# Performance work log

Hardware: AMD Instinct MI355X
Metric: run time of the kernel (lower is better)

The kernel has to match this reference:

```python
import jax, jax.numpy as jnp
import numpy as np

B, T, S, H = 4, 128, 512, 256


def setup_inputs() -> dict:
    key = jax.random.key(0)
    k0, k1, k2, k3, k4, k5, k6 = jax.random.split(key, 7)
    query = jax.random.normal(k0, (B, T, H), dtype=jnp.float32)
    encoder_outputs = jax.random.normal(k1, (B, S, H), dtype=jnp.float32)
    src_lengths = jax.random.randint(k2, (B,), 1, S + 1).astype(jnp.int32)
    # torch code's mask assumes max(src_lengths) == S (src dim of encoder_outputs)
    src_lengths = src_lengths.at[0].set(S)
    sc = np.float32(1.0 / np.sqrt(H))
    Ws = jax.random.normal(k3, (H, H), dtype=jnp.float32) * sc      # nn.Linear(H,H).weight
    Wh = jax.random.normal(k4, (H, H), dtype=jnp.float32) * sc
    v = jax.random.normal(k5, (H,), dtype=jnp.float32) * sc         # nn.Linear(H,1).weight squeezed
    Wout = jax.random.normal(k6, (H, 2 * H), dtype=jnp.float32) * sc
    return {"query": query, "encoder_outputs": encoder_outputs, "src_lengths": src_lengths,
            "Ws": Ws, "Wh": Wh, "v": v, "Wout": Wout}


def reference(query, encoder_outputs, src_lengths, Ws, Wh, v, Wout):
    # projections: torch Linear is x @ W.T
    pq = jnp.einsum('bth,oh->bto', query, Ws)             # (B,T,H)
    pe = jnp.einsum('bsh,oh->bso', encoder_outputs, Wh)   # (B,S,H)
    # additive score: v^T tanh(Ws q + Wh h) -> (B,T,S)
    e = jnp.einsum('btsh,h->bts', jnp.tanh(pq[:, :, None, :] + pe[:, None, :, :]), v)
    s = encoder_outputs.shape[1]
    mask = jnp.arange(s)[None, :] < src_lengths[:, None]  # (B,S) True = valid
    e = jnp.where(mask[:, None, :], e, -jnp.inf)
    alpha = jax.nn.softmax(e, axis=-1)                    # (B,T,S)
    c = jnp.einsum('bts,bsh->bth', alpha, encoder_outputs)  # context (B,T,H)
    cat = jnp.concatenate([query, c], axis=-1)            # (B,T,2H)
    attn_out = jnp.tanh(jnp.einsum('btf,of->bto', cat, Wout))
    return attn_out
```

## Files before the change

kernel.cpp:

```cpp
#include <hip/hip_runtime.h>
#include <math.h>

#define NB 4
#define NT 128
#define NS 512
#define NH 256

#define SCALE_2LOG2E 2.8853900817779268f

__device__ __forceinline__ float fast_exp2(float x) {
#if __has_builtin(__builtin_amdgcn_exp2f)
    return __builtin_amdgcn_exp2f(x);
#else
    return __expf(x * 0.6931471805599453f);
#endif
}

__device__ __forceinline__ float fast_tanh(float x) {
    float e = __expf(2.0f * x);
    return 1.0f - 2.0f / (e + 1.0f);
}

__device__ __forceinline__ float dot4(float4 a, float4 b, float acc) {
    acc = fmaf(a.x, b.x, acc);
    acc = fmaf(a.y, b.y, acc);
    acc = fmaf(a.z, b.z, acc);
    acc = fmaf(a.w, b.w, acc);
    return acc;
}

__device__ __forceinline__ void gemm_tile_64x64(
    float4* __restrict__ wsh, float4* __restrict__ xsh,
    const float* __restrict__ Wp, int wstride,
    const float* __restrict__ Xp,
    int kchunks, int tid, float acc[4][4])
{
    const int o0 = (tid & 15) * 4;
    const int m0 = (tid >> 4) * 4;
    const int srow = tid >> 2, sjl = tid & 3;
    const int wslotx = (tid & 7);
    const int xslotx = ((tid >> 4) & 7);

    for (int ck = 0; ck < kchunks; ++ck) {
        __syncthreads();
        {
            const float4* src = reinterpret_cast<const float4*>(
                Wp + (size_t)srow * wstride + ck * 128);
            const int rsw = (srow >> 2) & 7;
#pragma unroll
            for (int k = 0; k < 8; ++k) {
                const int j = sjl + 4 * k;
                wsh[srow * 32 + ((j & 31) ^ rsw)] = src[j];
            }
        }
        {
            const float4* src = reinterpret_cast<const float4*>(
                Xp + (size_t)srow * NH + ck * 128);
            const int rsw = (srow >> 2) & 7;
#pragma unroll
            for (int k = 0; k < 8; ++k) {
                const int j = sjl + 4 * k;
                xsh[srow * 32 + ((j & 31) ^ rsw)] = src[j];
            }
        }
        __syncthreads();

#pragma unroll 4
        for (int k4 = 0; k4 < 32; ++k4) {
            float4 wv0 = wsh[(o0 + 0) * 32 + (k4 ^ wslotx)];
            float4 wv1 = wsh[(o0 + 1) * 32 + (k4 ^ wslotx)];
            float4 wv2 = wsh[(o0 + 2) * 32 + (k4 ^ wslotx)];
            float4 wv3 = wsh[(o0 + 3) * 32 + (k4 ^ wslotx)];
            float4 xv0 = xsh[(m0 + 0) * 32 + (k4 ^ xslotx)];
            float4 xv1 = xsh[(m0 + 1) * 32 + (k4 ^ xslotx)];
            float4 xv2 = xsh[(m0 + 2) * 32 + (k4 ^ xslotx)];
            float4 xv3 = xsh[(m0 + 3) * 32 + (k4 ^ xslotx)];
            acc[0][0] = dot4(xv0, wv0, acc[0][0]);
            acc[0][1] = dot4(xv0, wv1, acc[0][1]);
            acc[0][2] = dot4(xv0, wv2, acc[0][2]);
            acc[0][3] = dot4(xv0, wv3, acc[0][3]);
            acc[1][0] = dot4(xv1, wv0, acc[1][0]);
            acc[1][1] = dot4(xv1, wv1, acc[1][1]);
            acc[1][2] = dot4(xv1, wv2, acc[1][2]);
            acc[1][3] = dot4(xv1, wv3, acc[1][3]);
            acc[2][0] = dot4(xv2, wv0, acc[2][0]);
            acc[2][1] = dot4(xv2, wv1, acc[2][1]);
            acc[2][2] = dot4(xv2, wv2, acc[2][2]);
            acc[2][3] = dot4(xv2, wv3, acc[2][3]);
            acc[3][0] = dot4(xv3, wv0, acc[3][0]);
            acc[3][1] = dot4(xv3, wv1, acc[3][1]);
            acc[3][2] = dot4(xv3, wv2, acc[3][2]);
            acc[3][3] = dot4(xv3, wv3, acc[3][3]);
        }
    }
}

__global__ __launch_bounds__(256) void kA_proj(
    const float* __restrict__ enc, const float* __restrict__ q,
    const float* __restrict__ Wh, const float* __restrict__ Ws,
    const float* __restrict__ Wout, const float* __restrict__ v,
    float4* __restrict__ peP, float* __restrict__ pq,
    float* __restrict__ oq, float* __restrict__ w2t, float* __restrict__ w)
{
    __shared__ float4 wsh[64 * 32];
    __shared__ float4 xsh[64 * 32];

    const int bx = blockIdx.x;
    const int tid = threadIdx.x;

    if (bx >= 192) {
        float* tl = reinterpret_cast<float*>(wsh);
        const int bi = bx - 192;
        const int oi = bi & 3, ki = bi >> 2;
        const int row = tid >> 2, jl = tid & 3;
        {
            const float4* src = reinterpret_cast<const float4*>(
                Wout + (size_t)(oi * 64 + row) * (2 * NH) + NH + ki * 64);
#pragma unroll
            for (int kk = 0; kk < 4; ++kk) {
                const int j = jl + 4 * kk;
                const float4 val = src[j];
                tl[(4 * j + 0) * 65 + row] = val.x;
                tl[(4 * j + 1) * 65 + row] = val.y;
                tl[(4 * j + 2) * 65 + row] = val.z;
                tl[(4 * j + 3) * 65 + row] = val.w;
            }
        }
        __syncthreads();
        {
#pragma unroll
            for (int kk = 0; kk < 4; ++kk) {
                const int j = jl + 4 * kk;
                float4 val;
                val.x = tl[row * 65 + 4 * j + 0];
                val.y = tl[row * 65 + 4 * j + 1];
                val.z = tl[row * 65 + 4 * j + 2];
                val.w = tl[row * 65 + 4 * j + 3];
                reinterpret_cast<float4*>(
                    w2t + (size_t)(ki * 64 + row) * NH + oi * 64)[j] = val;
            }
        }
        return;
    }

    float acc[4][4];
#pragma unroll
    for (int i = 0; i < 4; ++i)
#pragma unroll
        for (int j = 0; j < 4; ++j) acc[i][j] = 0.f;

    if (bx == 128) w[tid] = -2.0f * v[tid];

    const int o0 = (tid & 15) * 4;
    const int m0 = (tid >> 4) * 4;

    if (bx < 128) {
        const int mt = bx >> 2, ot = bx & 3;
        const int m_base = mt * 64;
        gemm_tile_64x64(wsh, xsh, Wh + (size_t)(ot * 64) * NH, NH,
                        enc + (size_t)m_base * NH, 2, tid, acc);
        const int b = m_base >> 9, s_base = m_base & (NS - 1);
        const int quad = ot * 16 + (tid & 15);
#pragma unroll
        for (int i = 0; i < 4; ++i) {
            peP[(size_t)(b * 64 + quad) * NS + s_base + m0 + i] =
                make_float4(acc[i][0] * SCALE_2LOG2E, acc[i][1] * SCALE_2LOG2E,
                            acc[i][2] * SCALE_2LOG2E, acc[i][3] * SCALE_2LOG2E);
        }
    } else if (bx < 160) {
        const int bi = bx - 128;
        const int mt = bi >> 2, ot = bi & 3;
        const int m_base = mt * 64;
        gemm_tile_64x64(wsh, xsh, Ws + (size_t)(ot * 64) * NH, NH,
                        q + (size_t)m_base * NH, 2, tid, acc);
#pragma unroll
        for (int i = 0; i < 4; ++i) {
            *reinterpret_cast<float4*>(
                pq + (size_t)(m_base + m0 + i) * NH + ot * 64 + o0) =
                make_float4(acc[i][0] * SCALE_2LOG2E, acc[i][1] * SCALE_2LOG2E,
                            acc[i][2] * SCALE_2LOG2E, acc[i][3] * SCALE_2LOG2E);
        }
    } else {
        const int bi = bx - 160;
        const int mt = bi >> 2, ot = bi & 3;
        const int m_base = mt * 64;
        gemm_tile_64x64(wsh, xsh, Wout + (size_t)(ot * 64) * (2 * NH), 2 * NH,
                        q + (size_t)m_base * NH, 2, tid, acc);
#pragma unroll
        for (int i = 0; i < 4; ++i) {
            *reinterpret_cast<float4*>(
                oq + (size_t)(m_base + m0 + i) * NH + ot * 64 + o0) =
                make_float4(acc[i][0], acc[i][1], acc[i][2], acc[i][3]);
        }
    }
}

__global__ __launch_bounds__(512) void kB_score(
    const float4* __restrict__ peP, const float* __restrict__ pq,
    const float* __restrict__ w, float* __restrict__ e)
{
    __shared__ float4 pp[64 * 64];
    __shared__ float4 pqs[16 * 64];
    __shared__ float4 wls[64];

    const int sx = blockIdx.x;
    const int ty = blockIdx.y;
    const int b  = blockIdx.z;
    const int tid = threadIdx.x;
    const int t0 = ty * 16;

    {
        const int row = tid >> 3, jl = tid & 7;
        const float4* src = peP + (size_t)(b * 64 + row) * NS + sx * 64;
#pragma unroll
        for (int k = 0; k < 8; ++k) pp[row * 64 + jl + 8 * k] = src[jl + 8 * k];
    }
    {
        const int r = tid >> 5, j = tid & 31;
        const float4* src = reinterpret_cast<const float4*>(
            pq + (size_t)(b * NT + t0 + r) * NH);
        pqs[r * 64 + j] = src[j];
        pqs[r * 64 + j + 32] = src[j + 32];
    }
    if (tid < 64) wls[tid] = reinterpret_cast<const float4*>(w)[tid];
    __syncthreads();

    const int lane = tid & 63;
    const int wvi  = tid >> 6;
    const int tA = wvi, tB = wvi + 8;

    float a0 = 0.f, a1 = 0.f, a2 = 0.f, a3 = 0.f;
    float b0 = 0.f, b1 = 0.f, b2 = 0.f, b3 = 0.f;
#pragma unroll 4
    for (int h4 = 0; h4 < 64; ++h4) {
        const float4 pv = pp[h4 * 64 + lane];
        const float4 qa = pqs[tA * 64 + h4];
        const float4 qb = pqs[tB * 64 + h4];
        const float4 wl = wls[h4];
        a0 = fmaf(wl.x, __builtin_amdgcn_rcpf(fast_exp2(pv.x + qa.x) + 1.0f), a0);
        a1 = fmaf(wl.y, __builtin_amdgcn_rcpf(fast_exp2(pv.y + qa.y) + 1.0f), a1);
        a2 = fmaf(wl.z, __builtin_amdgcn_rcpf(fast_exp2(pv.z + qa.z) + 1.0f), a2);
        a3 = fmaf(wl.w, __builtin_amdgcn_rcpf(fast_exp2(pv.w + qa.w) + 1.0f), a3);
        b0 = fmaf(wl.x, __builtin_amdgcn_rcpf(fast_exp2(pv.x + qb.x) + 1.0f), b0);
        b1 = fmaf(wl.y, __builtin_amdgcn_rcpf(fast_exp2(pv.y + qb.y) + 1.0f), b1);
        b2 = fmaf(wl.z, __builtin_amdgcn_rcpf(fast_exp2(pv.z + qb.z) + 1.0f), b2);
        b3 = fmaf(wl.w, __builtin_amdgcn_rcpf(fast_exp2(pv.w + qb.w) + 1.0f), b3);
    }
    e[(size_t)(b * NT + t0 + tA) * NS + sx * 64 + lane] = (a0 + a1) + (a2 + a3);
    e[(size_t)(b * NT + t0 + tB) * NS + sx * 64 + lane] = (b0 + b1) + (b2 + b3);
}

__global__ __launch_bounds__(512) void kC_ctx_out(
    const float* __restrict__ e, const float* __restrict__ enc,
    const int* __restrict__ lens, const float* __restrict__ w2t,
    const float* __restrict__ oq, float* __restrict__ out)
{
    __shared__ __align__(16) unsigned char smem[45088];
    float4* pt    = reinterpret_cast<float4*>(smem);
    float*  cpart = reinterpret_cast<float*>(smem + 8192);
    float4* opart = reinterpret_cast<float4*>(smem + 8192);
    float4* ct4   = reinterpret_cast<float4*>(smem + 40960);
    float*  rs    = reinterpret_cast<float*>(smem + 45056);

    const int tt = blockIdx.x;
    const int b  = blockIdx.y;
    const int tid = threadIdx.x;
    const int lane = tid & 63;
    const int wvi  = tid >> 6;
    const int tbase = tt * 4;
    const int len = lens[b];

    if (wvi < 4) {
        const int t = tbase + wvi;
        const float4* erow = reinterpret_cast<const float4*>(
            e + (size_t)(b * NT + t) * NS);
        float4 va = erow[lane];
        float4 vb = erow[lane + 64];
        const int c0 = 4 * lane, c1 = 256 + 4 * lane;
        if (c0 + 0 >= len) va.x = -INFINITY;
        if (c0 + 1 >= len) va.y = -INFINITY;
        if (c0 + 2 >= len) va.z = -INFINITY;
        if (c0 + 3 >= len) va.w = -INFINITY;
        if (c1 + 0 >= len) vb.x = -INFINITY;
        if (c1 + 1 >= len) vb.y = -INFINITY;
        if (c1 + 2 >= len) vb.z = -INFINITY;
        if (c1 + 3 >= len) vb.w = -INFINITY;

        float m = fmaxf(fmaxf(fmaxf(va.x, va.y), fmaxf(va.z, va.w)),
                        fmaxf(fmaxf(vb.x, vb.y), fmaxf(vb.z, vb.w)));
#pragma unroll
        for (int off = 32; off; off >>= 1) m = fmaxf(m, __shfl_xor(m, off));

        va.x = __expf(va.x - m); va.y = __expf(va.y - m);
        va.z = __expf(va.z - m); va.w = __expf(va.w - m);
        vb.x = __expf(vb.x - m); vb.y = __expf(vb.y - m);
        vb.z = __expf(vb.z - m); vb.w = __expf(vb.w - m);

        float sum = va.x + va.y + va.z + va.w + vb.x + vb.y + vb.z + vb.w;
#pragma unroll
        for (int off = 32; off; off >>= 1) sum += __shfl_xor(sum, off);
        if (lane == 0) rs[wvi] = 1.0f / sum;

        float* ptf = reinterpret_cast<float*>(pt);
        ptf[(c0 + 0) * 4 + wvi] = va.x;
        ptf[(c0 + 1) * 4 + wvi] = va.y;
        ptf[(c0 + 2) * 4 + wvi] = va.z;
        ptf[(c0 + 3) * 4 + wvi] = va.w;
        ptf[(c1 + 0) * 4 + wvi] = vb.x;
        ptf[(c1 + 1) * 4 + wvi] = vb.y;
        ptf[(c1 + 2) * 4 + wvi] = vb.z;
        ptf[(c1 + 3) * 4 + wvi] = vb.w;
    }
    __syncthreads();

    {
        const float4* enc4 = reinterpret_cast<const float4*>(
            enc + (size_t)b * NS * NH) + (size_t)wvi * 64 * 64 + lane;
        float4 ac0 = make_float4(0, 0, 0, 0), ac1 = ac0, ac2 = ac0, ac3 = ac0;
#pragma unroll 4
        for (int si = 0; si < 64; ++si) {
            const float4 xe = enc4[(size_t)si * 64];
            const float4 al = pt[wvi * 64 + si];
            ac0.x = fmaf(al.x, xe.x, ac0.x); ac0.y = fmaf(al.x, xe.y, ac0.y);
            ac0.z = fmaf(al.x, xe.z, ac0.z); ac0.w = fmaf(al.x, xe.w, ac0.w);
            ac1.x = fmaf(al.y, xe.x, ac1.x); ac1.y = fmaf(al.y, xe.y, ac1.y);
            ac1.z = fmaf(al.y, xe.z, ac1.z); ac1.w = fmaf(al.y, xe.w, ac1.w);
            ac2.x = fmaf(al.z, xe.x, ac2.x); ac2.y = fmaf(al.z, xe.y, ac2.y);
            ac2.z = fmaf(al.z, xe.z, ac2.z); ac2.w = fmaf(al.z, xe.w, ac2.w);
            ac3.x = fmaf(al.w, xe.x, ac3.x); ac3.y = fmaf(al.w, xe.y, ac3.y);
            ac3.z = fmaf(al.w, xe.z, ac3.z); ac3.w = fmaf(al.w, xe.w, ac3.w);
        }
        float4* cp = reinterpret_cast<float4*>(cpart);
        cp[(wvi * 4 + 0) * 64 + lane] = ac0;
        cp[(wvi * 4 + 1) * 64 + lane] = ac1;
        cp[(wvi * 4 + 2) * 64 + lane] = ac2;
        cp[(wvi * 4 + 3) * 64 + lane] = ac3;
    }
    __syncthreads();

    if (tid < 256) {
        const int h = tid;
        float v0 = 0.f, v1 = 0.f, v2 = 0.f, v3 = 0.f;
#pragma unroll
        for (int sg = 0; sg < 8; ++sg) {
            v0 += cpart[(sg * 4 + 0) * 256 + h];
            v1 += cpart[(sg * 4 + 1) * 256 + h];
            v2 += cpart[(sg * 4 + 2) * 256 + h];
            v3 += cpart[(sg * 4 + 3) * 256 + h];
        }
        ct4[h] = make_float4(v0 * rs[0], v1 * rs[1], v2 * rs[2], v3 * rs[3]);
    }
    __syncthreads();

    {
        const float4* w2t4 = reinterpret_cast<const float4*>(w2t);
        float4 op0 = make_float4(0, 0, 0, 0), op1 = op0, op2 = op0, op3 = op0;
#pragma unroll 4
        for (int hi = 0; hi < 32; ++hi) {
            const int h = wvi * 32 + hi;
            const float4 wv4 = w2t4[(size_t)h * 64 + lane];
            const float4 cl = ct4[h];
            op0.x = fmaf(cl.x, wv4.x, op0.x); op0.y = fmaf(cl.x, wv4.y, op0.y);
            op0.z = fmaf(cl.x, wv4.z, op0.z); op0.w = fmaf(cl.x, wv4.w, op0.w);
            op1.x = fmaf(cl.y, wv4.x, op1.x); op1.y = fmaf(cl.y, wv4.y, op1.y);
            op1.z = fmaf(cl.y, wv4.z, op1.z); op1.w = fmaf(cl.y, wv4.w, op1.w);
            op2.x = fmaf(cl.z, wv4.x, op2.x); op2.y = fmaf(cl.z, wv4.y, op2.y);
            op2.z = fmaf(cl.z, wv4.z, op2.z); op2.w = fmaf(cl.z, wv4.w, op2.w);
            op3.x = fmaf(cl.w, wv4.x, op3.x); op3.y = fmaf(cl.w, wv4.y, op3.y);
            op3.z = fmaf(cl.w, wv4.z, op3.z); op3.w = fmaf(cl.w, wv4.w, op3.w);
        }
        opart[(wvi * 4 + 0) * 64 + lane] = op0;
        opart[(wvi * 4 + 1) * 64 + lane] = op1;
        opart[(wvi * 4 + 2) * 64 + lane] = op2;
        opart[(wvi * 4 + 3) * 64 + lane] = op3;
    }
    __syncthreads();

    if (tid < 256) {
        const int o4 = tid & 63, tl = tid >> 6;
        float4 s = make_float4(0, 0, 0, 0);
#pragma unroll
        for (int kg = 0; kg < 8; ++kg) {
            const float4 p = opart[(kg * 4 + tl) * 64 + o4];
            s.x += p.x; s.y += p.y; s.z += p.z; s.w += p.w;
        }
        const int t = tbase + tl;
        const float4 qo = reinterpret_cast<const float4*>(
            oq + (size_t)(b * NT + t) * NH)[o4];
        float4 r;
        r.x = fast_tanh(s.x + qo.x);
        r.y = fast_tanh(s.y + qo.y);
        r.z = fast_tanh(s.z + qo.z);
        r.w = fast_tanh(s.w + qo.w);
        reinterpret_cast<float4*>(out + (size_t)(b * NT + t) * NH)[o4] = r;
    }
}

extern "C" void kernel_launch(void* const* d_in, const int* in_sizes, int n_in,
                              void* d_out, int out_size, void* d_ws, size_t ws_size,
                              hipStream_t stream) {
    const float* q    = (const float*)d_in[0];
    const float* enc  = (const float*)d_in[1];
    const int*   lens = (const int*)d_in[2];
    const float* Ws   = (const float*)d_in[3];
    const float* Wh   = (const float*)d_in[4];
    const float* v    = (const float*)d_in[5];
    const float* Wout = (const float*)d_in[6];
    float* out = (float*)d_out;

    float4* peP = (float4*)d_ws;
    float* pq  = (float*)d_ws + (size_t)NB * NH * NS;
    float* oq  = pq + (size_t)NB * NT * NH;
    float* w2t = oq + (size_t)NB * NT * NH;
    float* w   = w2t + (size_t)NH * NH;
    float* e   = w + NH;

    kA_proj<<<208, 256, 0, stream>>>(enc, q, Wh, Ws, Wout, v, peP, pq, oq, w2t, w);
    kB_score<<<dim3(8, 8, 4), 512, 0, stream>>>(peP, pq, w, e);
    kC_ctx_out<<<dim3(32, 4), 512, 0, stream>>>(e, enc, lens, w2t, oq, out);
}
```

Baseline: 45.49 us.

## Restructure projection kernel to stage full weight tile and stream activations from global

The projection kernel switches from a 64x64 two-operand shared-memory tiled GEMM to a scheme that stages a full 64-row weight slab (all 256 k) in shared memory once. Each thread then computes one output column for four rows, reading activations directly from global memory, broadcast across the wave. Blocks double to 400 with 512 threads each and tiles shrink to 32 rows, aiming for more parallelism and fewer barriers. The encoder projection output is transposed through a small shared buffer to keep the packed peP layout. In exchange, activation reuse now relies on cache rather than shared memory, and each output needs more global traffic.

```diff
diff --git a/kernel.cpp b/kernel.cpp
--- a/kernel.cpp
+++ b/kernel.cpp
@@ -29,113 +29,47 @@
     return acc;
 }
 
-__device__ __forceinline__ void gemm_tile_64x64(
-    float4* __restrict__ wsh, float4* __restrict__ xsh,
-    const float* __restrict__ Wp, int wstride,
-    const float* __restrict__ Xp,
-    int kchunks, int tid, float acc[4][4])
-{
-    const int o0 = (tid & 15) * 4;
-    const int m0 = (tid >> 4) * 4;
-    const int srow = tid >> 2, sjl = tid & 3;
-    const int wslotx = (tid & 7);
-    const int xslotx = ((tid >> 4) & 7);
-
-    for (int ck = 0; ck < kchunks; ++ck) {
-        __syncthreads();
-        {
-            const float4* src = reinterpret_cast<const float4*>(
-                Wp + (size_t)srow * wstride + ck * 128);
-            const int rsw = (srow >> 2) & 7;
-#pragma unroll
-            for (int k = 0; k < 8; ++k) {
-                const int j = sjl + 4 * k;
-                wsh[srow * 32 + ((j & 31) ^ rsw)] = src[j];
-            }
-        }
-        {
-            const float4* src = reinterpret_cast<const float4*>(
-                Xp + (size_t)srow * NH + ck * 128);
-            const int rsw = (srow >> 2) & 7;
-#pragma unroll
-            for (int k = 0; k < 8; ++k) {
-                const int j = sjl + 4 * k;
-                xsh[srow * 32 + ((j & 31) ^ rsw)] = src[j];
-            }
-        }
-        __syncthreads();
-
-#pragma unroll 4
-        for (int k4 = 0; k4 < 32; ++k4) {
-            float4 wv0 = wsh[(o0 + 0) * 32 + (k4 ^ wslotx)];
-            float4 wv1 = wsh[(o0 + 1) * 32 + (k4 ^ wslotx)];
-            float4 wv2 = wsh[(o0 + 2) * 32 + (k4 ^ wslotx)];
-            float4 wv3 = wsh[(o0 + 3) * 32 + (k4 ^ wslotx)];
-            float4 xv0 = xsh[(m0 + 0) * 32 + (k4 ^ xslotx)];
-            float4 xv1 = xsh[(m0 + 1) * 32 + (k4 ^ xslotx)];
-            float4 xv2 = xsh[(m0 + 2) * 32 + (k4 ^ xslotx)];
-            float4 xv3 = xsh[(m0 + 3) * 32 + (k4 ^ xslotx)];
-            acc[0][0] = dot4(xv0, wv0, acc[0][0]);
-            acc[0][1] = dot4(xv0, wv1, acc[0][1]);
-            acc[0][2] = dot4(xv0, wv2, acc[0][2]);
-            acc[0][3] = dot4(xv0, wv3, acc[0][3]);
-            acc[1][0] = dot4(xv1, wv0, acc[1][0]);
-            acc[1][1] = dot4(xv1, wv1, acc[1][1]);
-            acc[1][2] = dot4(xv1, wv2, acc[1][2]);
-            acc[1][3] = dot4(xv1, wv3, acc[1][3]);
-            acc[2][0] = dot4(xv2, wv0, acc[2][0]);
-            acc[2][1] = dot4(xv2, wv1, acc[2][1]);
-            acc[2][2] = dot4(xv2, wv2, acc[2][2]);
-            acc[2][3] = dot4(xv2, wv3, acc[2][3]);
-            acc[3][0] = dot4(xv3, wv0, acc[3][0]);
-            acc[3][1] = dot4(xv3, wv1, acc[3][1]);
-            acc[3][2] = dot4(xv3, wv2, acc[3][2]);
-            acc[3][3] = dot4(xv3, wv3, acc[3][3]);
-        }
-    }
-}
-
-__global__ __launch_bounds__(256) void kA_proj(
+__global__ __launch_bounds__(512) void kA_proj(
     const float* __restrict__ enc, const float* __restrict__ q,
     const float* __restrict__ Wh, const float* __restrict__ Ws,
     const float* __restrict__ Wout, const float* __restrict__ v,
     float4* __restrict__ peP, float* __restrict__ pq,
     float* __restrict__ oq, float* __restrict__ w2t, float* __restrict__ w)
 {
-    __shared__ float4 wsh[64 * 32];
-    __shared__ float4 xsh[64 * 32];
+    __shared__ float4 wsh[64 * 64];
+    __shared__ float tl[64 * 36];
 
     const int bx = blockIdx.x;
     const int tid = threadIdx.x;
 
-    if (bx >= 192) {
-        float* tl = reinterpret_cast<float*>(wsh);
-        const int bi = bx - 192;
+    if (bx >= 384) {
+        float* tlT = reinterpret_cast<float*>(wsh);
+        const int bi = bx - 384;
         const int oi = bi & 3, ki = bi >> 2;
-        const int row = tid >> 2, jl = tid & 3;
+        const int row = tid >> 3, jl = tid & 7;
         {
             const float4* src = reinterpret_cast<const float4*>(
                 Wout + (size_t)(oi * 64 + row) * (2 * NH) + NH + ki * 64);
 #pragma unroll
-            for (int kk = 0; kk < 4; ++kk) {
-                const int j = jl + 4 * kk;
+            for (int e2 = 0; e2 < 2; ++e2) {
+                const int j = jl * 2 + e2;
                 const float4 val = src[j];
-                tl[(4 * j + 0) * 65 + row] = val.x;
-                tl[(4 * j + 1) * 65 + row] = val.y;
-                tl[(4 * j + 2) * 65 + row] = val.z;
-                tl[(4 * j + 3) * 65 + row] = val.w;
+                tlT[(j * 4 + 0) * 65 + row] = val.x;
+                tlT[(j * 4 + 1) * 65 + row] = val.y;
+                tlT[(j * 4 + 2) * 65 + row] = val.z;
+                tlT[(j * 4 + 3) * 65 + row] = val.w;
             }
         }
         __syncthreads();
         {
 #pragma unroll
-            for (int kk = 0; kk < 4; ++kk) {
-                const int j = jl + 4 * kk;
+            for (int e2 = 0; e2 < 2; ++e2) {
+                const int j = jl * 2 + e2;
                 float4 val;
-                val.x = tl[row * 65 + 4 * j + 0];
-                val.y = tl[row * 65 + 4 * j + 1];
-                val.z = tl[row * 65 + 4 * j + 2];
-                val.w = tl[row * 65 + 4 * j + 3];
+                val.x = tlT[row * 65 + j * 4 + 0];
+                val.y = tlT[row * 65 + j * 4 + 1];
+                val.z = tlT[row * 65 + j * 4 + 2];
+                val.w = tlT[row * 65 + j * 4 + 3];
                 reinterpret_cast<float4*>(
                     w2t + (size_t)(ki * 64 + row) * NH + oi * 64)[j] = val;
             }
@@ -143,55 +77,75 @@
         return;
     }
 
-    float acc[4][4];
-#pragma unroll
-    for (int i = 0; i < 4; ++i)
-#pragma unroll
-        for (int j = 0; j < 4; ++j) acc[i][j] = 0.f;
-
-    if (bx == 128) w[tid] = -2.0f * v[tid];
-
-    const int o0 = (tid & 15) * 4;
-    const int m0 = (tid >> 4) * 4;
-
-    if (bx < 128) {
-        const int mt = bx >> 2, ot = bx & 3;
-        const int m_base = mt * 64;
-        gemm_tile_64x64(wsh, xsh, Wh + (size_t)(ot * 64) * NH, NH,
-                        enc + (size_t)m_base * NH, 2, tid, acc);
-        const int b = m_base >> 9, s_base = m_base & (NS - 1);
-        const int quad = ot * 16 + (tid & 15);
-#pragma unroll
-        for (int i = 0; i < 4; ++i) {
-            peP[(size_t)(b * 64 + quad) * NS + s_base + m0 + i] =
-                make_float4(acc[i][0] * SCALE_2LOG2E, acc[i][1] * SCALE_2LOG2E,
-                            acc[i][2] * SCALE_2LOG2E, acc[i][3] * SCALE_2LOG2E);
-        }
-    } else if (bx < 160) {
-        const int bi = bx - 128;
-        const int mt = bi >> 2, ot = bi & 3;
-        const int m_base = mt * 64;
-        gemm_tile_64x64(wsh, xsh, Ws + (size_t)(ot * 64) * NH, NH,
-                        q + (size_t)m_base * NH, 2, tid, acc);
-#pragma unroll
-        for (int i = 0; i < 4; ++i) {
-            *reinterpret_cast<float4*>(
-                pq + (size_t)(m_base + m0 + i) * NH + ot * 64 + o0) =
-                make_float4(acc[i][0] * SCALE_2LOG2E, acc[i][1] * SCALE_2LOG2E,
-                            acc[i][2] * SCALE_2LOG2E, acc[i][3] * SCALE_2LOG2E);
-        }
+    const float* X; const float* W; float* dst;
+    int r0, wstride, ot; float scale; bool is_pe = false;
+    if (bx < 256) {
+        const int mt = bx >> 2; ot = bx & 3;
+        X = enc; W = Wh; dst = nullptr; r0 = mt * 32; wstride = NH;
+        scale = SCALE_2LOG2E; is_pe = true;
+    } else if (bx < 320) {
+        const int bi = bx - 256; const int mt = bi >> 2; ot = bi & 3;
+        X = q; W = Ws; dst = pq; r0 = mt * 32; wstride = NH; scale = SCALE_2LOG2E;
+        if (bx == 256 && tid < NH) w[tid] = -2.0f * v[tid];
     } else {
-        const int bi = bx - 160;
-        const int mt = bi >> 2, ot = bi & 3;
-        const int m_base = mt * 64;
-        gemm_tile_64x64(wsh, xsh, Wout + (size_t)(ot * 64) * (2 * NH), 2 * NH,
-                        q + (size_t)m_base * NH, 2, tid, acc);
-#pragma unroll
-        for (int i = 0; i < 4; ++i) {
-            *reinterpret_cast<float4*>(
-                oq + (size_t)(m_base + m0 + i) * NH + ot * 64 + o0) =
-                make_float4(acc[i][0], acc[i][1], acc[i][2], acc[i][3]);
-        }
+        const int bi = bx - 320; const int mt = bi >> 2; ot = bi & 3;
+        X = q; W = Wout; dst = oq; r0 = mt * 32; wstride = 2 * NH; scale = 1.0f;
+    }
+
+    {
+        const int row = tid >> 3, jl = tid & 7;
+        const float4* src = reinterpret_cast<const float4*>(
+            W + (size_t)(ot * 64 + row) * wstride);
+        const int rsw = row & 7;
+#pragma unroll
+        for (int kk = 0; kk < 8; ++kk) {
+            const int j = jl + 8 * kk;
+            wsh[row * 64 + (j ^ rsw)] = src[j];
+        }
+    }
+    __syncthreads();
+
+    const int o = tid & 63;
+    const int wv = tid >> 6;
+    const int m0 = r0 + wv * 4;
+
+    const float4* __restrict__ x0 = reinterpret_cast<const float4*>(X + (size_t)(m0 + 0) * NH);
+    const float4* __restrict__ x1 = reinterpret_cast<const float4*>(X + (size_t)(m0 + 1) * NH);
+    const float4* __restrict__ x2 = reinterpret_cast<const float4*>(X + (size_t)(m0 + 2) * NH);
+    const float4* __restrict__ x3 = reinterpret_cast<const float4*>(X + (size_t)(m0 + 3) * NH);
+
+    float a0 = 0.f, a1 = 0.f, a2 = 0.f, a3 = 0.f;
+    const int osw = o & 7;
+#pragma unroll 4
+    for (int k4 = 0; k4 < 64; ++k4) {
+        const float4 wq = wsh[o * 64 + (k4 ^ osw)];
+        a0 = dot4(wq, x0[k4], a0);
+        a1 = dot4(wq, x1[k4], a1);
+        a2 = dot4(wq, x2[k4], a2);
+        a3 = dot4(wq, x3[k4], a3);
+    }
+    a0 *= scale; a1 *= scale; a2 *= scale; a3 *= scale;
+
+    if (!is_pe) {
+        const int oc = ot * 64 + o;
+        dst[(size_t)(m0 + 0) * NH + oc] = a0;
+        dst[(size_t)(m0 + 1) * NH + oc] = a1;
+        dst[(size_t)(m0 + 2) * NH + oc] = a2;
+        dst[(size_t)(m0 + 3) * NH + oc] = a3;
+    } else {
+        __syncthreads();
+        const int ml = wv * 4;
+        tl[o * 36 + ml + 0] = a0;
+        tl[o * 36 + ml + 1] = a1;
+        tl[o * 36 + ml + 2] = a2;
+        tl[o * 36 + ml + 3] = a3;
+        __syncthreads();
+        const int hq_l = tid >> 5, s_l = tid & 31;
+        const int b = r0 >> 9, s0 = r0 & (NS - 1);
+        const int base = 4 * hq_l * 36 + s_l;
+        const float4 v4 = make_float4(tl[base], tl[base + 36],
+                                      tl[base + 72], tl[base + 108]);
+        peP[((size_t)(b * 64 + ot * 16 + hq_l)) * NS + s0 + s_l] = v4;
     }
 }
 
@@ -377,14 +331,14 @@
     __syncthreads();
 
     if (tid < 256) {
-        const int o4 = tid & 63, tl = tid >> 6;
+        const int o4 = tid & 63, tl2 = tid >> 6;
         float4 s = make_float4(0, 0, 0, 0);
 #pragma unroll
         for (int kg = 0; kg < 8; ++kg) {
-            const float4 p = opart[(kg * 4 + tl) * 64 + o4];
+            const float4 p = opart[(kg * 4 + tl2) * 64 + o4];
             s.x += p.x; s.y += p.y; s.z += p.z; s.w += p.w;
         }
-        const int t = tbase + tl;
+        const int t = tbase + tl2;
         const float4 qo = reinterpret_cast<const float4*>(
             oq + (size_t)(b * NT + t) * NH)[o4];
         float4 r;
@@ -415,7 +369,7 @@
     float* w   = w2t + (size_t)NH * NH;
     float* e   = w + NH;
 
-    kA_proj<<<208, 256, 0, stream>>>(enc, q, Wh, Ws, Wout, v, peP, pq, oq, w2t, w);
+    kA_proj<<<400, 512, 0, stream>>>(enc, q, Wh, Ws, Wout, v, peP, pq, oq, w2t, w);
     kB_score<<<dim3(8, 8, 4), 512, 0, stream>>>(peP, pq, w, e);
     kC_ctx_out<<<dim3(32, 4), 512, 0, stream>>>(e, enc, lens, w2t, oq, out);
 }
```

After: 65.44 us. 43.8% more time.
